# Kernel optimization log

Measured on AMD Instinct MI355X. Metric: run time of the kernel, lower is better.

## Reference

```python
import jax, jax.numpy as jnp
import numpy as np

EPS = 1e-5   # torch F.layer_norm default eps
TOP_K = 20   # int(3*D^2 / (2*hr*N^2 + 10*D)) for D=768, N=196, hr=1.0
NUM_EXPERTS = 200  # 10 * TOP_K


def setup_inputs() -> dict:
    key = jax.random.key(0)
    ks = jax.random.split(key, 6)
    B, N, D = 32, 196, 768
    E, H = NUM_EXPERTS, 196  # H = int(N * hidden_ratio)
    s = 0.02
    return {
        "x": jax.random.normal(ks[0], (B, N, D), jnp.float32),
        "Wr": jax.random.normal(ks[1], (E, D), jnp.float32) * s,   # router.weight
        "W1": jax.random.normal(ks[2], (E, H, N), jnp.float32) * s,  # fc1.weight per expert
        "b1": jnp.zeros((E, H), jnp.float32),
        "W2": jax.random.normal(ks[3], (E, N, H), jnp.float32) * s,  # fc2.weight per expert
        "b2": jnp.zeros((E, N), jnp.float32),
        "Wo": jax.random.normal(ks[4], (D, D), jnp.float32) * s,     # out_proj.weight
        "bo": jnp.zeros((D,), jnp.float32),
    }


def reference(x, Wr, W1, b1, W2, b2, Wo, bo):
    B, N, D = x.shape
    E = Wr.shape[0]
    K = TOP_K

    # Router: per-sample routing on token-mean features
    logits = x.mean(axis=1) @ Wr.T                      # (B, E)
    probs = jax.nn.softmax(logits, axis=-1)             # (B, E)
    w, idx = jax.lax.top_k(probs, K)                    # (B, K) sorted desc, as torch.topk
    w = w / w.sum(axis=-1, keepdims=True)               # renormalize top-k weights

    # TokenMixer operates in (B, D, N) space: layernorm over tokens (no affine),
    # then fc1 (N->H), gelu(tanh), fc2 (H->N).
    xt = jnp.swapaxes(x, 1, 2)                          # (B, D, N)
    mu = xt.mean(axis=-1, keepdims=True)
    var = xt.var(axis=-1, keepdims=True)                # population var (matches F.layer_norm)
    z = (xt - mu) * jax.lax.rsqrt(var + EPS)            # (B, D, N)

    # Gather each sample's K expert weight matrices and batch the MLPs.
    W1g, b1g = W1[idx], b1[idx]                         # (B,K,H,N), (B,K,H)
    W2g, b2g = W2[idx], b2[idx]                         # (B,K,N,H), (B,K,N)

    h = jnp.einsum('bdn,bkhn->bkdh', z, W1g) + b1g[:, :, None, :]
    a = jax.nn.gelu(h, approximate=True)                # tanh-approx GELU
    o = jnp.einsum('bkdh,bknh->bkdn', a, W2g) + b2g[:, :, None, :]

    # Weighted combine over the K selected experts, back to (B, N, D)
    mix = jnp.einsum('bk,bkdn->bnd', w, o)

    out = mix @ Wo.T + bo                               # out_proj

    # Load-balancing aux loss (top-1 assignment fraction vs mean router prob)
    top1 = jax.nn.one_hot(idx[:, 0], E, dtype=probs.dtype)   # (B, E)
    aux = E * jnp.sum(probs.mean(axis=0) * top1.mean(axis=0))
    return out, aux
```

## Files before the change

### kernel.cpp

```cpp
#include <hip/hip_runtime.h>
#include <math.h>

constexpr int B  = 32;
constexpr int N  = 196;
constexpr int D  = 768;
constexpr int E  = 200;
constexpr int TK = 20;

constexpr int NGRP = 4;
constexpr int PRB  = 14336;
constexpr int EXB  = 114688;
constexpr int LK   = 40;

typedef __bf16 bf16x8 __attribute__((ext_vector_type(8)));
typedef __bf16 bf16x4 __attribute__((ext_vector_type(4)));
typedef float  f32x4  __attribute__((ext_vector_type(4)));
typedef long   longx2 __attribute__((ext_vector_type(2)));
typedef unsigned char uchar;

#define GLDS16(gp, lp)                                                        \
  __builtin_amdgcn_global_load_lds(                                           \
      (const __attribute__((address_space(1))) void*)(gp),                    \
      (__attribute__((address_space(3))) void*)(lp), 16, 0, 0)

#define WAITVM12  __builtin_amdgcn_s_waitcnt(0x0F7C)
#define WAITVM8   __builtin_amdgcn_s_waitcnt(0x0F78)
#define WAITVM0   __builtin_amdgcn_s_waitcnt(0x0F70)
#define WAITLGKM0 __builtin_amdgcn_s_waitcnt(0xC07F)
#define BAR       __builtin_amdgcn_s_barrier()

__device__ __forceinline__ float gelu_fast(float x) {
  float u = x * fmaf(x * x, 0.044715f, 1.0f);
  float e = exp2f(-2.3022084f * u);
  return x * __builtin_amdgcn_rcpf(1.0f + e);
}

__device__ __forceinline__ uchar f32_to_f8(float v) {
  return (uchar)(__builtin_amdgcn_cvt_pk_fp8_f32(v, v, 0, false) & 0xff);
}

__global__ __launch_bounds__(256) void k_ln(const float* __restrict__ x,
                                            uchar* __restrict__ zb,
                                            float* __restrict__ mu) {
  int b = blockIdx.x / 12, dt = blockIdx.x % 12;
  int d0 = dt * 64;
  int t = threadIdx.x;
  int q = t >> 6, d = t & 63;
  __shared__ float ps[256], pq[256];
  __shared__ float ms[64], rss[64];
  __shared__ alignas(16) uchar zt[64 * 256];

  for (int i = t; i < 1024; i += 256) ((uint4*)zt)[i] = (uint4){0, 0, 0, 0};

  const float* xp = x + ((size_t)b * N + q * 49) * D + d0 + d;
  float s = 0.f, sq = 0.f;
  #pragma unroll 7
  for (int n = 0; n < 49; ++n) {
    float v = xp[(size_t)n * D];
    s += v; sq += v * v;
  }
  ps[t] = s; pq[t] = sq;
  __syncthreads();
  if (t < 64) {
    float S = ps[t] + ps[t + 64] + ps[t + 128] + ps[t + 192];
    float Q = pq[t] + pq[t + 64] + pq[t + 128] + pq[t + 192];
    float m = S * (1.0f / N);
    float var = Q * (1.0f / N) - m * m;
    ms[t] = m; rss[t] = rsqrtf(var + 1e-5f);
    mu[(size_t)b * D + d0 + t] = m;
  }
  __syncthreads();
  float m = ms[d], r = rss[d];
  int dsw = (d >> 1) & 3;
  #pragma unroll 7
  for (int n = 0; n < 49; ++n) {
    float v = xp[(size_t)n * D];
    int tok = q * 49 + n;
    int qp = ((tok >> 3) & 3) ^ dsw;
    int off = d * 256 + (tok >> 6) * 64 + qp * 16 + ((tok >> 5) & 1) * 8 + (tok & 7);
    zt[off] = f32_to_f8((v - m) * r);
  }
  __syncthreads();
  #pragma unroll
  for (int pair = 0; pair < 4; ++pair) {
    uint4* dst = (uint4*)(zb + (((size_t)b * 4 + pair) * 768 + d0) * 64);
    dst[t] = ((const uint4*)zt)[(t >> 2) * 16 + pair * 4 + (t & 3)];
  }
}

__global__ __launch_bounds__(256) void k_convert(
    const float* __restrict__ W1, const float* __restrict__ W2,
    const float* __restrict__ Wo,
    uchar* __restrict__ Wf, __bf16* __restrict__ Wob) {
  int bx = blockIdx.x;
  int t = threadIdx.x;
  if (bx >= 400) {
    int i = (bx - 400) * 256 + t;
    float4 v = *(const float4*)&Wo[(size_t)i * 4];
    bf16x4 o = {(__bf16)v.x, (__bf16)v.y, (__bf16)v.z, (__bf16)v.w};
    *(bf16x4*)&Wob[(size_t)i * 4] = o;
    return;
  }
  int e = bx >> 1, mat = bx & 1;
  __shared__ alignas(16) uchar ls[224 * 256];
  for (int i = t; i < 3584; i += 256) ((uint4*)ls)[i] = (uint4){0, 0, 0, 0};
  __syncthreads();
  const float* src = (mat ? W2 : W1) + (size_t)e * 196 * 196;
  for (int i = t; i < 196 * 49; i += 256) {
    int r = i / 49, c4 = (i - r * 49) * 4;
    float4 v = *(const float4*)&src[(size_t)r * 196 + c4];
    int lo = __builtin_amdgcn_cvt_pk_fp8_f32(v.x, v.y, 0, false);
    unsigned int pk = (unsigned int)__builtin_amdgcn_cvt_pk_fp8_f32(v.z, v.w, lo, true);
    *(unsigned int*)&ls[r * 256 + c4] = pk;
  }
  __syncthreads();
  uchar* dst = Wf + (size_t)e * EXB + mat * 4 * PRB;
  for (int s = t; s < 3584; s += 256) {
    int p = s / 896, rem = s - p * 896;
    int col = rem >> 2, qp = rem & 3;
    int ql = qp ^ ((col >> 1) & 3);
    unsigned long lo = *(const unsigned long*)&ls[col * 256 + p * 64 + ql * 8];
    unsigned long hi = *(const unsigned long*)&ls[col * 256 + p * 64 + 32 + ql * 8];
    longx2 o; o[0] = (long)lo; o[1] = (long)hi;
    *(longx2*)&dst[(size_t)s * 16] = o;
  }
}

__global__ void k_router(const float* __restrict__ mu, const float* __restrict__ Wr,
                         float* __restrict__ probs, int* __restrict__ idxg,
                         float* __restrict__ wg) {
  int b = blockIdx.x;
  int t = threadIdx.x;
  __shared__ float smu[768];
  __shared__ float sp[E];
  __shared__ float smax, ssum;
  __shared__ float svals[TK];
  __shared__ int   sidx[TK];

  for (int i = t; i < 768; i += 256) smu[i] = mu[(size_t)b * D + i];
  __syncthreads();

  float logit = 0.f;
  if (t < E) {
    const float4* wr4 = (const float4*)(Wr + (size_t)t * D);
    const float4* m4  = (const float4*)smu;
    float acc = 0.f;
    #pragma unroll 4
    for (int i = 0; i < 192; ++i) {
      float4 w = wr4[i], m = m4[i];
      acc = fmaf(w.x, m.x, acc); acc = fmaf(w.y, m.y, acc);
      acc = fmaf(w.z, m.z, acc); acc = fmaf(w.w, m.w, acc);
    }
    logit = acc;
    sp[t] = acc;
  }
  __syncthreads();
  if (t == 0) {
    float mx = sp[0];
    for (int e = 1; e < E; ++e) mx = fmaxf(mx, sp[e]);
    smax = mx;
  }
  __syncthreads();
  if (t < E) sp[t] = expf(logit - smax);
  __syncthreads();
  if (t == 0) {
    float s = 0.f;
    for (int e = 0; e < E; ++e) s += sp[e];
    ssum = s;
  }
  __syncthreads();
  if (t < E) {
    sp[t] = sp[t] / ssum;
    probs[(size_t)b * E + t] = sp[t];
  }
  __syncthreads();

  for (int k = 0; k < TK; ++k) {
    if (t < 64) {
      float bv = -1e30f; int bi = 0;
      for (int e = t; e < E; e += 64) {
        float v = sp[e];
        if (v > bv) { bv = v; bi = e; }
      }
      #pragma unroll
      for (int off = 32; off > 0; off >>= 1) {
        float ov = __shfl_down(bv, off);
        int   oi = __shfl_down(bi, off);
        if (ov > bv || (ov == bv && oi < bi)) { bv = ov; bi = oi; }
      }
      if (t == 0) {
        svals[k] = bv; sidx[k] = bi;
        sp[bi] = -2e30f;
      }
    }
    __syncthreads();
  }
  if (t == 0) {
    float s = 0.f;
    for (int k = 0; k < TK; ++k) s += svals[k];
    float inv = 1.0f / s;
    for (int k = 0; k < TK; ++k) {
      wg[b * TK + k]   = svals[k] * inv;
      idxg[b * TK + k] = sidx[k];
    }
  }
}

__global__ __launch_bounds__(256, 2) void k_expert(
    const uchar* __restrict__ zb, const uchar* __restrict__ Wf,
    const float* __restrict__ b1, const float* __restrict__ b2,
    const int* __restrict__ idxg, const float* __restrict__ wg,
    __bf16* __restrict__ mixg) {
  __shared__ alignas(16) uchar pool[75776];
  __shared__ alignas(16) __bf16 b1s[5 * 196];
  __shared__ alignas(16) __bf16 b2s[5 * 196];
  __shared__ int   eidx_s[5];
  __shared__ float w_s[5];
  uchar* zs  = pool;
  uchar* at  = pool + 16384;
  uchar* wsb = pool + 32768;
  __bf16* tb = (__bf16*)pool;

  int xw = blockIdx.x & 7, rr_ = blockIdx.x >> 3;
  int j = rr_ / 12, dt = rr_ - j * 12;
  int gid = j * 8 + xw;
  int g = gid & 3, b = gid >> 2;
  int d0 = dt * 64;

  int t = threadIdx.x;
  int lane = t & 63, wave = t >> 6;
  int quad = lane >> 4, l16 = lane & 15;
  int wrow = (wave & 1) * 32;
  int wcol = (wave >> 1) * 112;
  int qp = quad ^ ((l16 >> 1) & 3);

  if (t < 5) {
    eidx_s[t] = idxg[b * TK + g * 5 + t];
    w_s[t]    = wg[b * TK + g * 5 + t];
  }
  for (int i = t; i < 980; i += 256) {
    int kk = i / 196, col = i - kk * 196;
    int ee = idxg[b * TK + g * 5 + kk];
    b1s[i] = (__bf16)b1[ee * 196 + col];
    b2s[i] = (__bf16)b2[ee * 196 + col];
  }
  *(unsigned long*)&at[3 * 4096 + (t >> 2) * 64 + (t & 3) * 16 + 8] = 0ul;
  __syncthreads();

  {
    const uchar* zbase = zb + ((size_t)b * 4 * 768 + d0) * 64;
    #pragma unroll
    for (int p = 0; p < 4; ++p)
      GLDS16(zbase + (size_t)p * (768 * 64) + t * 16, zs + p * 4096 + t * 16);
  }

  int s0 = t * 16, s1 = (t + 256) * 16, s2 = (t + 512) * 16;
  int s3 = ((t & 127) + 768) * 16;

  auto issue = [&](int qn) {
    int qq = qn > 39 ? 39 : qn;
    int kk2 = qq >> 3, rem = qq & 7;
    const uchar* src = Wf + (size_t)eidx_s[kk2] * EXB + rem * PRB;
    uchar* lb = wsb + (qn % 3) * PRB;
    GLDS16(src + s0, lb + s0);
    GLDS16(src + s1, lb + s1);
    GLDS16(src + s2, lb + s2);
    GLDS16(src + s3, lb + s3);
  };
  issue(0); issue(1); issue(2);

  WAITVM12;
  BAR;
  longx2 zf[4][2];
  #pragma unroll
  for (int p = 0; p < 4; ++p) {
    zf[p][0] = *(const longx2*)&zs[p * 4096 + (wrow + l16) * 64 + qp * 16];
    zf[p][1] = *(const longx2*)&zs[p * 4096 + (wrow + 16 + l16) * 64 + qp * 16];
  }

  f32x4 macc[14];
  #pragma unroll
  for (int i = 0; i < 14; ++i) macc[i] = (f32x4){0.f, 0.f, 0.f, 0.f};

  #pragma unroll 1
  for (int kk = 0; kk < 5; ++kk) {
    float wkv = w_s[kk];
    f32x4 hacc[14];
    #pragma unroll
    for (int i = 0; i < 14; ++i) hacc[i] = (f32x4){0.f, 0.f, 0.f, 0.f};

    #pragma unroll 1
    for (int p = 0; p < 4; ++p) {
      int q = kk * 8 + p;
      WAITVM8;
      BAR;
      const uchar* buf = wsb + (q % 3) * PRB;
      #pragma unroll
      for (int ct = 0; ct < 7; ++ct) {
        longx2 bf = *(const longx2*)&buf[(wcol + ct * 16 + l16) * 64 + qp * 16];
        hacc[ct]     = __builtin_amdgcn_mfma_f32_16x16x32_fp8_fp8(bf[0], zf[p][0][0], hacc[ct], 0, 0, 0);
        hacc[ct]     = __builtin_amdgcn_mfma_f32_16x16x32_fp8_fp8(bf[1], zf[p][0][1], hacc[ct], 0, 0, 0);
        hacc[7 + ct] = __builtin_amdgcn_mfma_f32_16x16x32_fp8_fp8(bf[0], zf[p][1][0], hacc[7 + ct], 0, 0, 0);
        hacc[7 + ct] = __builtin_amdgcn_mfma_f32_16x16x32_fp8_fp8(bf[1], zf[p][1][1], hacc[7 + ct], 0, 0, 0);
      }
      BAR;
      issue(q + 3);
    }

    #pragma unroll
    for (int ct = 0; ct < 7; ++ct) {
      int hb = wcol + ct * 16 + quad * 4;
      bool valid = hb < 196;
      unsigned pk0 = 0u, pk1 = 0u;
      if (valid) {
        bf16x4 b4 = *(const bf16x4*)&b1s[kk * 196 + hb];
        float bv0 = (float)b4[0], bv1 = (float)b4[1];
        float bv2 = (float)b4[2], bv3 = (float)b4[3];
        f32x4 h0 = hacc[ct], h1 = hacc[7 + ct];
        pk0 = (unsigned)__builtin_amdgcn_cvt_pk_fp8_f32(
                  gelu_fast(h0[0] + bv0) * wkv, gelu_fast(h0[1] + bv1) * wkv, 0, false);
        pk0 = (unsigned)__builtin_amdgcn_cvt_pk_fp8_f32(
                  gelu_fast(h0[2] + bv2) * wkv, gelu_fast(h0[3] + bv3) * wkv, (int)pk0, true);
        pk1 = (unsigned)__builtin_amdgcn_cvt_pk_fp8_f32(
                  gelu_fast(h1[0] + bv0) * wkv, gelu_fast(h1[1] + bv1) * wkv, 0, false);
        pk1 = (unsigned)__builtin_amdgcn_cvt_pk_fp8_f32(
                  gelu_fast(h1[2] + bv2) * wkv, gelu_fast(h1[3] + bv3) * wkv, (int)pk1, true);
      }
      int d0r = wrow + l16;
      int addr0 = (hb >> 6) * 4096 + d0r * 64 + ((((hb >> 3) & 3) ^ ((d0r >> 1) & 3)) << 4)
                + ((hb >> 5) & 1) * 8 + (quad & 1) * 4;
      *(unsigned*)&at[addr0]        = pk0;
      *(unsigned*)&at[addr0 + 1024] = pk1;
    }
    WAITLGKM0;

    #pragma unroll 1
    for (int p = 0; p < 4; ++p) {
      int q = kk * 8 + 4 + p;
      WAITVM8;
      BAR;
      const uchar* buf = wsb + (q % 3) * PRB;
      longx2 a0 = *(const longx2*)&at[p * 4096 + (wrow + l16) * 64 + qp * 16];
      longx2 a1 = *(const longx2*)&at[p * 4096 + (wrow + 16 + l16) * 64 + qp * 16];
      #pragma unroll
      for (int ct = 0; ct < 7; ++ct) {
        longx2 bf = *(const longx2*)&buf[(wcol + ct * 16 + l16) * 64 + qp * 16];
        macc[ct]     = __builtin_amdgcn_mfma_f32_16x16x32_fp8_fp8(a0[0], bf[0], macc[ct], 0, 0, 0);
        macc[ct]     = __builtin_amdgcn_mfma_f32_16x16x32_fp8_fp8(a0[1], bf[1], macc[ct], 0, 0, 0);
        macc[7 + ct] = __builtin_amdgcn_mfma_f32_16x16x32_fp8_fp8(a1[0], bf[0], macc[7 + ct], 0, 0, 0);
        macc[7 + ct] = __builtin_amdgcn_mfma_f32_16x16x32_fp8_fp8(a1[1], bf[1], macc[7 + ct], 0, 0, 0);
      }
      BAR;
      issue(q + 3);
    }
  }

  WAITVM0;
  BAR;
  #pragma unroll
  for (int ct = 0; ct < 7; ++ct) {
    int ncol = wcol + ct * 16 + l16;
    float bsum = 0.f;
    if (ncol < 196) {
      #pragma unroll
      for (int k5 = 0; k5 < 5; ++k5)
        bsum += w_s[k5] * (float)b2s[k5 * 196 + ncol];
    }
    #pragma unroll
    for (int rt = 0; rt < 2; ++rt) {
      f32x4 v = macc[rt * 7 + ct];
      bf16x4 o = {(__bf16)(v[0] + bsum), (__bf16)(v[1] + bsum),
                  (__bf16)(v[2] + bsum), (__bf16)(v[3] + bsum)};
      *(bf16x4*)&tb[ncol * 68 + wrow + rt * 16 + quad * 4] = o;
    }
  }
  __syncthreads();
  __bf16* mp = mixg + ((size_t)(g * B + b) * N) * D + d0;
  #pragma unroll
  for (int i = 0; i < 7; ++i) {
    int s = i * 256 + t;
    if (s < 1568) {
      int n = s >> 3, c = s & 7;
      const uint2* pa = (const uint2*)&tb[n * 68 + c * 8];
      uint2 v0 = pa[0], v1 = pa[1];
      uint4 v = {v0.x, v0.y, v1.x, v1.y};
      *(uint4*)&mp[(size_t)n * D + c * 8] = v;
    }
  }
}

__global__ __launch_bounds__(256, 2) void k_outproj(
    const __bf16* __restrict__ mixg, const __bf16* __restrict__ Wob,
    const float* __restrict__ bo, const float* __restrict__ probs,
    const int* __restrict__ idxg, float* __restrict__ out,
    float* __restrict__ out_aux) {
  __shared__ alignas(16) __bf16 As[64 * LK];
  __shared__ alignas(16) __bf16 Bs[256 * LK];
  const size_t GS = (size_t)B * N * D;

  int t = threadIdx.x;
  if (blockIdx.x == 0 && t < 32) {
    int top1 = idxg[t * TK];
    float s = 0.f;
    for (int bb = 0; bb < B; ++bb) s += probs[(size_t)bb * E + top1];
    #pragma unroll
    for (int off = 16; off > 0; off >>= 1) s += __shfl_down(s, off);
    if (t == 0) out_aux[0] = s * ((float)E / ((float)B * (float)B));
  }

  int m0 = (blockIdx.x % 98) * 64;
  int e0 = (blockIdx.x / 98) * 256;
  int lane = t & 63, wave = t >> 6;
  int quad = lane >> 4, l16 = lane & 15;
  int wrow = (wave & 1) * 32;
  int wcol = (wave >> 1) * 128;
  int arow = t >> 2, ach = t & 3;
  const __bf16* ap0 = mixg + (size_t)(m0 + arow) * D + ach * 8;

  f32x4 acc[16];
  #pragma unroll
  for (int i = 0; i < 16; ++i) acc[i] = (f32x4){0.f, 0.f, 0.f, 0.f};

  const uint4* wsrc = (const uint4*)Wob;
  #pragma unroll 1
  for (int c = 0; c < 24; ++c) {
    int k0 = c * 32;
    __syncthreads();
    {
      const __bf16* ap = ap0 + k0;
      bf16x8 g0 = *(const bf16x8*)(ap);
      bf16x8 g1 = *(const bf16x8*)(ap + GS);
      bf16x8 g2 = *(const bf16x8*)(ap + 2 * GS);
      bf16x8 g3 = *(const bf16x8*)(ap + 3 * GS);
      bf16x8 r;
      #pragma unroll
      for (int jj = 0; jj < 8; ++jj)
        r[jj] = (__bf16)((float)g0[jj] + (float)g1[jj] + (float)g2[jj] + (float)g3[jj]);
      *(bf16x8*)&As[arow * LK + ach * 8] = r;
    }
    for (int p = t; p < 1024; p += 256) {
      int rr = p >> 2, sub = p & 3;
      uint4 v = wsrc[(((size_t)(e0 + rr)) * D + k0) / 8 + sub];
      *(uint4*)&Bs[rr * LK + sub * 8] = v;
    }
    __syncthreads();
    bf16x8 a0 = *(const bf16x8*)&As[(wrow + l16) * LK + quad * 8];
    bf16x8 a1 = *(const bf16x8*)&As[(wrow + 16 + l16) * LK + quad * 8];
    #pragma unroll
    for (int ct = 0; ct < 8; ++ct) {
      bf16x8 bfr = *(const bf16x8*)&Bs[(wcol + ct * 16 + l16) * LK + quad * 8];
      acc[ct]     = __builtin_amdgcn_mfma_f32_16x16x32_bf16(a0, bfr, acc[ct], 0, 0, 0);
      acc[8 + ct] = __builtin_amdgcn_mfma_f32_16x16x32_bf16(a1, bfr, acc[8 + ct], 0, 0, 0);
    }
  }

  #pragma unroll
  for (int ct = 0; ct < 8; ++ct) {
    int e = e0 + wcol + ct * 16 + l16;
    float bov = bo[e];
    #pragma unroll
    for (int rt = 0; rt < 2; ++rt) {
      #pragma unroll
      for (int rx = 0; rx < 4; ++rx) {
        int m = m0 + wrow + rt * 16 + quad * 4 + rx;
        out[(size_t)m * D + e] = acc[rt * 8 + ct][rx] + bov;
      }
    }
  }
}

extern "C" void kernel_launch(void* const* d_in, const int* in_sizes, int n_in,
                              void* d_out, int out_size, void* d_ws, size_t ws_size,
                              hipStream_t stream) {
  const float* x  = (const float*)d_in[0];
  const float* Wr = (const float*)d_in[1];
  const float* W1 = (const float*)d_in[2];
  const float* b1 = (const float*)d_in[3];
  const float* W2 = (const float*)d_in[4];
  const float* b2 = (const float*)d_in[5];
  const float* Wo = (const float*)d_in[6];
  const float* bo = (const float*)d_in[7];
  float* out = (float*)d_out;

  char* p = (char*)d_ws;
  auto alloc = [&](size_t bytes) {
    char* r = p;
    p += (bytes + 255) & ~(size_t)255;
    return r;
  };
  uchar*  zb   = (uchar*)alloc((size_t)B * 4 * 768 * 64);
  float*  mu   = (float*)alloc((size_t)B * D * 4);
  uchar*  Wf   = (uchar*)alloc((size_t)E * EXB);
  __bf16* Wob  = (__bf16*)alloc((size_t)D * D * 2);
  __bf16* mixg = (__bf16*)alloc((size_t)NGRP * B * N * D * 2);
  float*  probs= (float*)alloc((size_t)B * E * 4);
  int*    idxg = (int*)alloc((size_t)B * TK * 4);
  float*  wg   = (float*)alloc((size_t)B * TK * 4);

  k_ln<<<dim3(B * 12), dim3(256), 0, stream>>>(x, zb, mu);
  k_convert<<<dim3(976), dim3(256), 0, stream>>>(W1, W2, Wo, Wf, Wob);
  k_router<<<dim3(B), dim3(256), 0, stream>>>(mu, Wr, probs, idxg, wg);
  k_expert<<<dim3(1536), dim3(256), 0, stream>>>(zb, Wf, b1, b2, idxg, wg, mixg);
  k_outproj<<<dim3(294), dim3(256), 0, stream>>>(mixg, Wob, bo, probs, idxg,
                                                 out, out + (size_t)B * N * D);
}
```

Before: 394.9 us.

## Split expert tiles across 8 waves and halve out-projection row tiles

The expert kernel moves to 512-thread blocks with eight waves, each owning 16 rows instead of 32. This halves per-wave accumulators and fragments, and the weight-tile copies are re-split across twice as many threads with adjusted waitcnt thresholds. MFMA sections are bracketed with s_setprio to favour issue of matrix instructions. The out-projection uses 32-row tiles and twice the blocks, aiming for more parallelism, at the cost of less reuse per loaded Wo tile and more barrier pressure.

After: 394.5 us. No clear change (-0.1%).

```diff
diff --git a/kernel.cpp b/kernel.cpp
--- a/kernel.cpp
+++ b/kernel.cpp
@@ -23,8 +23,8 @@
       (const __attribute__((address_space(1))) void*)(gp),                    \
       (__attribute__((address_space(3))) void*)(lp), 16, 0, 0)
 
-#define WAITVM12  __builtin_amdgcn_s_waitcnt(0x0F7C)
-#define WAITVM8   __builtin_amdgcn_s_waitcnt(0x0F78)
+#define WAITVM6   __builtin_amdgcn_s_waitcnt(0x0F76)
+#define WAITVM4   __builtin_amdgcn_s_waitcnt(0x0F74)
 #define WAITVM0   __builtin_amdgcn_s_waitcnt(0x0F70)
 #define WAITLGKM0 __builtin_amdgcn_s_waitcnt(0xC07F)
 #define BAR       __builtin_amdgcn_s_barrier()
@@ -206,7 +206,7 @@
   }
 }
 
-__global__ __launch_bounds__(256, 2) void k_expert(
+__global__ __launch_bounds__(512, 4) void k_expert(
     const uchar* __restrict__ zb, const uchar* __restrict__ Wf,
     const float* __restrict__ b1, const float* __restrict__ b2,
     const int* __restrict__ idxg, const float* __restrict__ wg,
@@ -230,32 +230,36 @@
   int t = threadIdx.x;
   int lane = t & 63, wave = t >> 6;
   int quad = lane >> 4, l16 = lane & 15;
-  int wrow = (wave & 1) * 32;
-  int wcol = (wave >> 1) * 112;
+  int wrow = (wave & 3) * 16;
+  int wcol = (wave >> 2) * 112;
   int qp = quad ^ ((l16 >> 1) & 3);
 
   if (t < 5) {
     eidx_s[t] = idxg[b * TK + g * 5 + t];
     w_s[t]    = wg[b * TK + g * 5 + t];
   }
-  for (int i = t; i < 980; i += 256) {
+  for (int i = t; i < 980; i += 512) {
     int kk = i / 196, col = i - kk * 196;
     int ee = idxg[b * TK + g * 5 + kk];
     b1s[i] = (__bf16)b1[ee * 196 + col];
     b2s[i] = (__bf16)b2[ee * 196 + col];
   }
-  *(unsigned long*)&at[3 * 4096 + (t >> 2) * 64 + (t & 3) * 16 + 8] = 0ul;
+  if (t < 256)
+    *(unsigned long*)&at[3 * 4096 + (t >> 2) * 64 + (t & 3) * 16 + 8] = 0ul;
   __syncthreads();
 
   {
     const uchar* zbase = zb + ((size_t)b * 4 * 768 + d0) * 64;
     #pragma unroll
-    for (int p = 0; p < 4; ++p)
-      GLDS16(zbase + (size_t)p * (768 * 64) + t * 16, zs + p * 4096 + t * 16);
-  }
-
-  int s0 = t * 16, s1 = (t + 256) * 16, s2 = (t + 512) * 16;
-  int s3 = ((t & 127) + 768) * 16;
+    for (int i = 0; i < 2; ++i) {
+      int s = i * 512 + t;
+      int p = s >> 8, w = s & 255;
+      GLDS16(zbase + (size_t)p * (768 * 64) + w * 16, zs + p * 4096 + w * 16);
+    }
+  }
+
+  int s0 = t * 16;
+  int s1 = (t < 384) ? (512 + t) * 16 : (t - 384) * 16;
 
   auto issue = [&](int qn) {
     int qq = qn > 39 ? 39 : qn;
@@ -264,45 +268,41 @@
     uchar* lb = wsb + (qn % 3) * PRB;
     GLDS16(src + s0, lb + s0);
     GLDS16(src + s1, lb + s1);
-    GLDS16(src + s2, lb + s2);
-    GLDS16(src + s3, lb + s3);
   };
   issue(0); issue(1); issue(2);
 
-  WAITVM12;
+  WAITVM6;
   BAR;
-  longx2 zf[4][2];
-  #pragma unroll
-  for (int p = 0; p < 4; ++p) {
-    zf[p][0] = *(const longx2*)&zs[p * 4096 + (wrow + l16) * 64 + qp * 16];
-    zf[p][1] = *(const longx2*)&zs[p * 4096 + (wrow + 16 + l16) * 64 + qp * 16];
-  }
-
-  f32x4 macc[14];
-  #pragma unroll
-  for (int i = 0; i < 14; ++i) macc[i] = (f32x4){0.f, 0.f, 0.f, 0.f};
+  longx2 zf[4];
+  #pragma unroll
+  for (int p = 0; p < 4; ++p)
+    zf[p] = *(const longx2*)&zs[p * 4096 + (wrow + l16) * 64 + qp * 16];
+
+  f32x4 macc[7];
+  #pragma unroll
+  for (int i = 0; i < 7; ++i) macc[i] = (f32x4){0.f, 0.f, 0.f, 0.f};
 
   #pragma unroll 1
   for (int kk = 0; kk < 5; ++kk) {
     float wkv = w_s[kk];
-    f32x4 hacc[14];
-    #pragma unroll
-    for (int i = 0; i < 14; ++i) hacc[i] = (f32x4){0.f, 0.f, 0.f, 0.f};
+    f32x4 hacc[7];
+    #pragma unroll
+    for (int i = 0; i < 7; ++i) hacc[i] = (f32x4){0.f, 0.f, 0.f, 0.f};
 
     #pragma unroll 1
     for (int p = 0; p < 4; ++p) {
       int q = kk * 8 + p;
-      WAITVM8;
+      WAITVM4;
       BAR;
       const uchar* buf = wsb + (q % 3) * PRB;
+      __builtin_amdgcn_s_setprio(1);
       #pragma unroll
       for (int ct = 0; ct < 7; ++ct) {
         longx2 bf = *(const longx2*)&buf[(wcol + ct * 16 + l16) * 64 + qp * 16];
-        hacc[ct]     = __builtin_amdgcn_mfma_f32_16x16x32_fp8_fp8(bf[0], zf[p][0][0], hacc[ct], 0, 0, 0);
-        hacc[ct]     = __builtin_amdgcn_mfma_f32_16x16x32_fp8_fp8(bf[1], zf[p][0][1], hacc[ct], 0, 0, 0);
-        hacc[7 + ct] = __builtin_amdgcn_mfma_f32_16x16x32_fp8_fp8(bf[0], zf[p][1][0], hacc[7 + ct], 0, 0, 0);
-        hacc[7 + ct] = __builtin_amdgcn_mfma_f32_16x16x32_fp8_fp8(bf[1], zf[p][1][1], hacc[7 + ct], 0, 0, 0);
-      }
+        hacc[ct] = __builtin_amdgcn_mfma_f32_16x16x32_fp8_fp8(bf[0], zf[p][0], hacc[ct], 0, 0, 0);
+        hacc[ct] = __builtin_amdgcn_mfma_f32_16x16x32_fp8_fp8(bf[1], zf[p][1], hacc[ct], 0, 0, 0);
+      }
+      __builtin_amdgcn_s_setprio(0);
       BAR;
       issue(q + 3);
     }
@@ -311,45 +311,39 @@
     for (int ct = 0; ct < 7; ++ct) {
       int hb = wcol + ct * 16 + quad * 4;
       bool valid = hb < 196;
-      unsigned pk0 = 0u, pk1 = 0u;
+      unsigned pk0 = 0u;
       if (valid) {
         bf16x4 b4 = *(const bf16x4*)&b1s[kk * 196 + hb];
-        float bv0 = (float)b4[0], bv1 = (float)b4[1];
-        float bv2 = (float)b4[2], bv3 = (float)b4[3];
-        f32x4 h0 = hacc[ct], h1 = hacc[7 + ct];
+        f32x4 h0 = hacc[ct];
         pk0 = (unsigned)__builtin_amdgcn_cvt_pk_fp8_f32(
-                  gelu_fast(h0[0] + bv0) * wkv, gelu_fast(h0[1] + bv1) * wkv, 0, false);
+                  gelu_fast(h0[0] + (float)b4[0]) * wkv,
+                  gelu_fast(h0[1] + (float)b4[1]) * wkv, 0, false);
         pk0 = (unsigned)__builtin_amdgcn_cvt_pk_fp8_f32(
-                  gelu_fast(h0[2] + bv2) * wkv, gelu_fast(h0[3] + bv3) * wkv, (int)pk0, true);
-        pk1 = (unsigned)__builtin_amdgcn_cvt_pk_fp8_f32(
-                  gelu_fast(h1[0] + bv0) * wkv, gelu_fast(h1[1] + bv1) * wkv, 0, false);
-        pk1 = (unsigned)__builtin_amdgcn_cvt_pk_fp8_f32(
-                  gelu_fast(h1[2] + bv2) * wkv, gelu_fast(h1[3] + bv3) * wkv, (int)pk1, true);
+                  gelu_fast(h0[2] + (float)b4[2]) * wkv,
+                  gelu_fast(h0[3] + (float)b4[3]) * wkv, (int)pk0, true);
       }
       int d0r = wrow + l16;
       int addr0 = (hb >> 6) * 4096 + d0r * 64 + ((((hb >> 3) & 3) ^ ((d0r >> 1) & 3)) << 4)
                 + ((hb >> 5) & 1) * 8 + (quad & 1) * 4;
-      *(unsigned*)&at[addr0]        = pk0;
-      *(unsigned*)&at[addr0 + 1024] = pk1;
+      *(unsigned*)&at[addr0] = pk0;
     }
     WAITLGKM0;
 
     #pragma unroll 1
     for (int p = 0; p < 4; ++p) {
       int q = kk * 8 + 4 + p;
-      WAITVM8;
+      WAITVM4;
       BAR;
       const uchar* buf = wsb + (q % 3) * PRB;
       longx2 a0 = *(const longx2*)&at[p * 4096 + (wrow + l16) * 64 + qp * 16];
-      longx2 a1 = *(const longx2*)&at[p * 4096 + (wrow + 16 + l16) * 64 + qp * 16];
+      __builtin_amdgcn_s_setprio(1);
       #pragma unroll
       for (int ct = 0; ct < 7; ++ct) {
         longx2 bf = *(const longx2*)&buf[(wcol + ct * 16 + l16) * 64 + qp * 16];
-        macc[ct]     = __builtin_amdgcn_mfma_f32_16x16x32_fp8_fp8(a0[0], bf[0], macc[ct], 0, 0, 0);
-        macc[ct]     = __builtin_amdgcn_mfma_f32_16x16x32_fp8_fp8(a0[1], bf[1], macc[ct], 0, 0, 0);
-        macc[7 + ct] = __builtin_amdgcn_mfma_f32_16x16x32_fp8_fp8(a1[0], bf[0], macc[7 + ct], 0, 0, 0);
-        macc[7 + ct] = __builtin_amdgcn_mfma_f32_16x16x32_fp8_fp8(a1[1], bf[1], macc[7 + ct], 0, 0, 0);
-      }
+        macc[ct] = __builtin_amdgcn_mfma_f32_16x16x32_fp8_fp8(a0[0], bf[0], macc[ct], 0, 0, 0);
+        macc[ct] = __builtin_amdgcn_mfma_f32_16x16x32_fp8_fp8(a0[1], bf[1], macc[ct], 0, 0, 0);
+      }
+      __builtin_amdgcn_s_setprio(0);
       BAR;
       issue(q + 3);
     }
@@ -366,19 +360,16 @@
       for (int k5 = 0; k5 < 5; ++k5)
         bsum += w_s[k5] * (float)b2s[k5 * 196 + ncol];
     }
-    #pragma unroll
-    for (int rt = 0; rt < 2; ++rt) {
-      f32x4 v = macc[rt * 7 + ct];
-      bf16x4 o = {(__bf16)(v[0] + bsum), (__bf16)(v[1] + bsum),
-                  (__bf16)(v[2] + bsum), (__bf16)(v[3] + bsum)};
-      *(bf16x4*)&tb[ncol * 68 + wrow + rt * 16 + quad * 4] = o;
-    }
+    f32x4 v = macc[ct];
+    bf16x4 o = {(__bf16)(v[0] + bsum), (__bf16)(v[1] + bsum),
+                (__bf16)(v[2] + bsum), (__bf16)(v[3] + bsum)};
+    *(bf16x4*)&tb[ncol * 68 + wrow + quad * 4] = o;
   }
   __syncthreads();
   __bf16* mp = mixg + ((size_t)(g * B + b) * N) * D + d0;
   #pragma unroll
-  for (int i = 0; i < 7; ++i) {
-    int s = i * 256 + t;
+  for (int i = 0; i < 4; ++i) {
+    int s = i * 512 + t;
     if (s < 1568) {
       int n = s >> 3, c = s & 7;
       const uint2* pa = (const uint2*)&tb[n * 68 + c * 8];
@@ -394,7 +385,7 @@
     const float* __restrict__ bo, const float* __restrict__ probs,
     const int* __restrict__ idxg, float* __restrict__ out,
     float* __restrict__ out_aux) {
-  __shared__ alignas(16) __bf16 As[64 * LK];
+  __shared__ alignas(16) __bf16 As[32 * LK];
   __shared__ alignas(16) __bf16 Bs[256 * LK];
   const size_t GS = (size_t)B * N * D;
 
@@ -408,25 +399,25 @@
     if (t == 0) out_aux[0] = s * ((float)E / ((float)B * (float)B));
   }
 
-  int m0 = (blockIdx.x % 98) * 64;
-  int e0 = (blockIdx.x / 98) * 256;
+  int m0 = (blockIdx.x % 196) * 32;
+  int e0 = (blockIdx.x / 196) * 256;
   int lane = t & 63, wave = t >> 6;
   int quad = lane >> 4, l16 = lane & 15;
-  int wrow = (wave & 1) * 32;
+  int wrow = (wave & 1) * 16;
   int wcol = (wave >> 1) * 128;
   int arow = t >> 2, ach = t & 3;
-  const __bf16* ap0 = mixg + (size_t)(m0 + arow) * D + ach * 8;
-
-  f32x4 acc[16];
-  #pragma unroll
-  for (int i = 0; i < 16; ++i) acc[i] = (f32x4){0.f, 0.f, 0.f, 0.f};
+  const __bf16* ap0 = mixg + (size_t)(m0 + (arow & 31)) * D + ach * 8;
+
+  f32x4 acc[8];
+  #pragma unroll
+  for (int i = 0; i < 8; ++i) acc[i] = (f32x4){0.f, 0.f, 0.f, 0.f};
 
   const uint4* wsrc = (const uint4*)Wob;
   #pragma unroll 1
   for (int c = 0; c < 24; ++c) {
     int k0 = c * 32;
     __syncthreads();
-    {
+    if (t < 128) {
       const __bf16* ap = ap0 + k0;
       bf16x8 g0 = *(const bf16x8*)(ap);
       bf16x8 g1 = *(const bf16x8*)(ap + GS);
@@ -445,12 +436,10 @@
     }
     __syncthreads();
     bf16x8 a0 = *(const bf16x8*)&As[(wrow + l16) * LK + quad * 8];
-    bf16x8 a1 = *(const bf16x8*)&As[(wrow + 16 + l16) * LK + quad * 8];
     #pragma unroll
     for (int ct = 0; ct < 8; ++ct) {
       bf16x8 bfr = *(const bf16x8*)&Bs[(wcol + ct * 16 + l16) * LK + quad * 8];
-      acc[ct]     = __builtin_amdgcn_mfma_f32_16x16x32_bf16(a0, bfr, acc[ct], 0, 0, 0);
-      acc[8 + ct] = __builtin_amdgcn_mfma_f32_16x16x32_bf16(a1, bfr, acc[8 + ct], 0, 0, 0);
+      acc[ct] = __builtin_amdgcn_mfma_f32_16x16x32_bf16(a0, bfr, acc[ct], 0, 0, 0);
     }
   }
 
@@ -459,12 +448,9 @@
     int e = e0 + wcol + ct * 16 + l16;
     float bov = bo[e];
     #pragma unroll
-    for (int rt = 0; rt < 2; ++rt) {
-      #pragma unroll
-      for (int rx = 0; rx < 4; ++rx) {
-        int m = m0 + wrow + rt * 16 + quad * 4 + rx;
-        out[(size_t)m * D + e] = acc[rt * 8 + ct][rx] + bov;
-      }
+    for (int rx = 0; rx < 4; ++rx) {
+      int m = m0 + wrow + quad * 4 + rx;
+      out[(size_t)m * D + e] = acc[ct][rx] + bov;
     }
   }
 }
@@ -500,7 +486,7 @@
   k_ln<<<dim3(B * 12), dim3(256), 0, stream>>>(x, zb, mu);
   k_convert<<<dim3(976), dim3(256), 0, stream>>>(W1, W2, Wo, Wf, Wob);
   k_router<<<dim3(B), dim3(256), 0, stream>>>(mu, Wr, probs, idxg, wg);
-  k_expert<<<dim3(1536), dim3(256), 0, stream>>>(zb, Wf, b1, b2, idxg, wg, mixg);
-  k_outproj<<<dim3(294), dim3(256), 0, stream>>>(mixg, Wob, bo, probs, idxg,
+  k_expert<<<dim3(1536), dim3(512), 0, stream>>>(zb, Wf, b1, b2, idxg, wg, mixg);
+  k_outproj<<<dim3(588), dim3(256), 0, stream>>>(mixg, Wob, bo, probs, idxg,
                                                  out, out + (size_t)B * N * D);
 }
```
